# Kernel tuning notes

Measured on AMD Instinct MI355X. Metric: run time of the kernel, lower is better.

The kernel has to match this reference:

```python
import jax, jax.numpy as jnp
import numpy as np

HEADS = 8

def _rotate_every_two(t):
    # t: [..., d]; interleaved rotation (-x2, x1) pairs
    x1 = t[..., ::2]
    x2 = t[..., 1::2]
    return jnp.stack([-x2, x1], axis=-1).reshape(t.shape)

def _theta_shift(t, sin, cos):
    return t * cos + _rotate_every_two(t) * sin

def setup_inputs() -> dict:
    key = jax.random.key(0)
    ks = jax.random.split(key, 5)
    B, H, W, C = 4, 40, 40, 512
    dh = C // HEADS
    x = jax.random.normal(ks[0], (B, H, W, C), dtype=jnp.float32)
    sin = jax.random.normal(ks[1], (H, W, dh), dtype=jnp.float32)
    cos = jax.random.normal(ks[2], (H, W, dh), dtype=jnp.float32)
    # 1x1 conv weight [3C, C] (kernel dims squeezed) + bias
    w_qkv = jax.random.normal(ks[3], (3 * C, C), dtype=jnp.float32) * (C ** -0.5)
    b_qkv = jnp.zeros((3 * C,), dtype=jnp.float32)
    return {"x": x, "sin": sin, "cos": cos, "w_qkv": w_qkv, "b_qkv": b_qkv}

def reference(x, sin, cos, w_qkv, b_qkv):
    B, H, W, C = x.shape
    heads = HEADS
    dh = C // heads
    scale = dh ** -0.5
    # 1x1 conv == per-pixel linear projection
    qkv = jnp.einsum('bhwc,oc->bhwo', x, w_qkv) + b_qkv  # [B,H,W,3C]
    q, k, v = jnp.split(qkv, 3, axis=-1)

    def to_heads(t):
        # channel order is (heads, dim_head) per the torch rearrange
        return t.reshape(B, H, W, heads, dh).transpose(0, 3, 1, 2, 4)  # [B,heads,H,W,dh]

    q = _theta_shift(to_heads(q), sin, cos)
    k = _theta_shift(to_heads(k), sin, cos)
    # v is computed but unused downstream in the original module (bug preserved)

    N = H * W
    q = q.reshape(B, heads, N, dh)
    k = k.reshape(B, heads, N, dh)

    attn = jnp.einsum('bhnd,bhmd->bhnm', q, k) * scale  # [B,heads,N,N]
    p = jax.nn.softmax(attn, axis=-1)
    # NOTE: original code does matmul(logist, kfine_heads) — K, not V. Kept faithful.
    out = jnp.einsum('bhnm,bhmd->bhnd', p, k)  # [B,heads,N,dh]
    out = out.transpose(0, 2, 1, 3).reshape(B, H, W, C)
    return out
```

## Files before the change

### kernel.cpp

```cpp
#include <hip/hip_runtime.h>
#include <hip/hip_bf16.h>


typedef __hip_bfloat16 bf16;
typedef __attribute__((ext_vector_type(8))) short short8;
typedef __attribute__((ext_vector_type(4))) short bfx4;
typedef __attribute__((ext_vector_type(4))) float f32x4;

#define NSP 1600
#define CDIM 512
#define DH 64

__device__ __forceinline__ f32x4 mfma32(short8 a, short8 b, f32x4 c) {
  return __builtin_amdgcn_mfma_f32_16x16x32_bf16(a, b, c, 0, 0, 0);
}

#if __has_builtin(__builtin_amdgcn_mfma_f32_16x16x16bf16_1k)
__device__ __forceinline__ f32x4 mfma_k16(bfx4 a, bfx4 b, f32x4 c) {
  return __builtin_amdgcn_mfma_f32_16x16x16bf16_1k(a, b, c, 0, 0, 0);
}
#else
__device__ __forceinline__ f32x4 mfma_k16(bfx4 a, bfx4 b, f32x4 c) {
  short8 a8 = {a.x, a.y, a.z, a.w, 0, 0, 0, 0};
  short8 b8 = {b.x, b.y, b.z, b.w, 0, 0, 0, 0};
  return __builtin_amdgcn_mfma_f32_16x16x32_bf16(a8, b8, c, 0, 0, 0);
}
#endif

__device__ __forceinline__ short8 cvt8(float4 v0, float4 v1) {
  short8 r; bf16* p = (bf16*)&r;
  p[0] = __float2bfloat16(v0.x); p[1] = __float2bfloat16(v0.y);
  p[2] = __float2bfloat16(v0.z); p[3] = __float2bfloat16(v0.w);
  p[4] = __float2bfloat16(v1.x); p[5] = __float2bfloat16(v1.y);
  p[6] = __float2bfloat16(v1.z); p[7] = __float2bfloat16(v1.w);
  return r;
}

extern "C" __global__ __launch_bounds__(256)
void cvt_kernel(const float* __restrict__ x, const float* __restrict__ w,
                const float* __restrict__ sin_t, const float* __restrict__ cos_t,
                bf16* __restrict__ x_bf, bf16* __restrict__ w_bf,
                float* __restrict__ sinT, float* __restrict__ cosT)
{
  __shared__ float t_lds[64][68];
  const int bid = blockIdx.x, tid = threadIdx.x;
  if (bid < 1600) {
    const size_t i = (size_t)bid * 2048 + tid * 8;
    float4 v0 = *(const float4*)(x + i);
    float4 v1 = *(const float4*)(x + i + 4);
    *(short8*)(x_bf + i) = cvt8(v0, v1);
  } else if (bid < 1856) {
    const size_t i = (size_t)(bid - 1600) * 2048 + tid * 8;
    float4 v0 = *(const float4*)(w + i);
    float4 v1 = *(const float4*)(w + i + 4);
    *(short8*)(w_bf + i) = cvt8(v0, v1);
  } else {
    const int t = bid - 1856;
    const float* src = (t < 25) ? sin_t : cos_t;
    float* dst = (t < 25) ? sinT : cosT;
    const int nt = (t < 25) ? t : t - 25;
    const int r = tid >> 2, c = (tid & 3) * 16;
#pragma unroll
    for (int j = 0; j < 4; ++j)
      *(float4*)&t_lds[r][c + j * 4] =
          *(const float4*)(src + (size_t)(nt * 64 + r) * 64 + c + j * 4);
    __syncthreads();
#pragma unroll
    for (int j4 = 0; j4 < 4; ++j4) {
      float4 o;
      o.x = t_lds[c + j4 * 4 + 0][r];
      o.y = t_lds[c + j4 * 4 + 1][r];
      o.z = t_lds[c + j4 * 4 + 2][r];
      o.w = t_lds[c + j4 * 4 + 3][r];
      *(float4*)(dst + (size_t)r * NSP + nt * 64 + c + j4 * 4) = o;
    }
  }
}

extern "C" __global__ __launch_bounds__(256)
void proj_kernel(const bf16* __restrict__ x_bf, const bf16* __restrict__ w_bf,
                 const float* __restrict__ bias, const float* __restrict__ sinT,
                 const float* __restrict__ cosT, bf16* __restrict__ q_ws,
                 bf16* __restrict__ k2_ws, bf16* __restrict__ kt2_ws)
{
  __shared__ __align__(16) char smem[36864];
  bf16 (*x_lds)[72] = (bf16(*)[72])smem;
  bf16 (*w_lds)[72] = (bf16(*)[72])(smem + 18432);
  bf16* ep = (bf16*)smem;

  const int tid  = threadIdx.x;
  const int wave = tid >> 6;
  const int lane = tid & 63;
  const int col  = lane & 15;
  const int quad = lane >> 4;
  const int wm = wave >> 1, wo = wave & 1;
  const int m0 = blockIdx.x * 128;
  const int o0 = blockIdx.y * 128;

  f32x4 acc[4][4];
#pragma unroll
  for (int i = 0; i < 4; ++i)
#pragma unroll
    for (int j = 0; j < 4; ++j) acc[i][j] = {0.f, 0.f, 0.f, 0.f};

  const int srow = tid >> 1;
  const int sch  = (tid & 1) * 32;

  for (int kt = 0; kt < 8; ++kt) {
    __syncthreads();
    {
      const bf16* xs = x_bf + (size_t)(m0 + srow) * CDIM + kt * 64 + sch;
      const bf16* ws = w_bf + (size_t)(o0 + srow) * CDIM + kt * 64 + sch;
#pragma unroll
      for (int j = 0; j < 4; ++j) {
        *(short8*)&x_lds[srow][sch + j * 8] = *(const short8*)(xs + j * 8);
        *(short8*)&w_lds[srow][sch + j * 8] = *(const short8*)(ws + j * 8);
      }
    }
    __syncthreads();
#pragma unroll
    for (int half = 0; half < 2; ++half) {
      short8 af[4], bfr[4];
#pragma unroll
      for (int mt = 0; mt < 4; ++mt)
        af[mt] = *(short8*)&x_lds[wm * 64 + mt * 16 + col][half * 32 + quad * 8];
#pragma unroll
      for (int ot = 0; ot < 4; ++ot)
        bfr[ot] = *(short8*)&w_lds[wo * 64 + ot * 16 + col][half * 32 + quad * 8];
#pragma unroll
      for (int mt = 0; mt < 4; ++mt)
#pragma unroll
        for (int ot = 0; ot < 4; ++ot)
          acc[mt][ot] = mfma32(af[mt], bfr[ot], acc[mt][ot]);
    }
  }

  __syncthreads();
  const int b_idx = (m0 + wm * 64) / NSP;
  const int n0w   = m0 + wm * 64 - b_idx * NSP;
  const bool isq  = (o0 < 512);
#pragma unroll
  for (int ot = 0; ot < 4; ++ot) {
    const int o_local = wo * 64 + ot * 16 + col;
    const int o_g = o0 + o_local;
    const float bv = bias[o_g];
    const int d = o_g & 63;
#pragma unroll
    for (int mt = 0; mt < 4; ++mt) {
      const int nl = mt * 16 + quad * 4;
      float t[4], rot[4];
#pragma unroll
      for (int r = 0; r < 4; ++r) t[r] = acc[mt][ot][r] + bv;
#pragma unroll
      for (int r = 0; r < 4; ++r) {
        float tp = __shfl_xor(t[r], 1, 64);
        rot[r] = (lane & 1) ? tp : -tp;
      }
      const float4 c4 = *(const float4*)(cosT + (size_t)d * NSP + n0w + nl);
      const float4 s4 = *(const float4*)(sinT + (size_t)d * NSP + n0w + nl);
      float res[4];
      res[0] = t[0] * c4.x + rot[0] * s4.x;
      res[1] = t[1] * c4.y + rot[1] * s4.y;
      res[2] = t[2] * c4.z + rot[2] * s4.z;
      res[3] = t[3] * c4.w + rot[3] * s4.w;
      if (isq) {
#pragma unroll
        for (int r = 0; r < 4; ++r) res[r] *= 0.125f;
      }
      bfx4 pk; bf16* pp = (bf16*)&pk;
#pragma unroll
      for (int r = 0; r < 4; ++r) pp[r] = __float2bfloat16(res[r]);
      *(bfx4*)&ep[o_local * 132 + wm * 64 + nl] = pk;
    }
  }
  __syncthreads();

  if (isq) {
    const int m_l = tid >> 1, half = tid & 1;
    const int gm = m0 + m_l;
    const int bi = gm / NSP, n = gm - bi * NSP;
    const int h = (o0 >> 6) + half;
    bf16* base = q_ws + ((size_t)(bi * 8 + h) * NSP + n) * 64;
#pragma unroll
    for (int c = 0; c < 8; ++c) {
      short8 v; bf16* vp = (bf16*)&v;
#pragma unroll
      for (int j = 0; j < 8; ++j) vp[j] = ep[(half * 64 + c * 8 + j) * 132 + m_l];
      *(short8*)(base + c * 8) = v;
    }
  } else {
    const int h0 = (o0 - 512) >> 6;
#pragma unroll
    for (int it = 0; it < 8; ++it) {
      const int ci = it * 256 + tid;
      const int hh = ci >> 10, T = (ci >> 9) & 1, inner = ci & 511;
      const int ccol = inner & 15, cq = (inner >> 4) & 3;
      const int f = (inner >> 6) & 1, ti = (inner >> 7) & 1, kh2 = (inner >> 8) & 1;
      const int gmb = m0 + T * 64;
      const int bi = gmb / NSP, ktile = (gmb - bi * NSP) >> 6;
      const int m_l = T * 64 + (2 * kh2 + ti) * 16 + ccol;
      const int er0 = hh * 64 + (f * 4 + cq) * 8;
      short8 v; bf16* vp = (bf16*)&v;
#pragma unroll
      for (int j = 0; j < 8; ++j) vp[j] = ep[(er0 + j) * 132 + m_l];
      *(short8*)(k2_ws +
          (((size_t)(bi * 8 + h0 + hh) * 25 + ktile) * 512 + inner) * 8) = v;
    }
#pragma unroll
    for (int it = 0; it < 8; ++it) {
      const int ci = it * 256 + tid;
      const int hh = ci >> 10, T = (ci >> 9) & 1, inner = ci & 511;
      const int ccol = inner & 15, cq = (inner >> 4) & 3;
      const int dt = (inner >> 6) & 3, kh2 = (inner >> 8) & 1;
      const int gmb = m0 + T * 64;
      const int bi = gmb / NSP, ktile = (gmb - bi * NSP) >> 6;
      const bf16* eprow =
          ep + (hh * 64 + dt * 16 + ccol) * 132 + T * 64 + kh2 * 32 + cq * 4;
      short8 v;
      ((bfx4*)&v)[0] = *(const bfx4*)(eprow);
      ((bfx4*)&v)[1] = *(const bfx4*)(eprow + 16);
      *(short8*)(kt2_ws +
          (((size_t)(bi * 8 + h0 + hh) * 25 + ktile) * 512 + inner) * 8) = v;
    }
  }
}


#define LOADF(KF, KTF, KT)                                                    \
  {                                                                           \
    const bf16* kc_  = k2b  + (KT) * 4096;                                    \
    const bf16* kc2_ = kt2b + (KT) * 4096;                                    \
    _Pragma("unroll")                                                         \
    for (int ti = 0; ti < 2; ++ti)                                            \
      _Pragma("unroll")                                                       \
      for (int f = 0; f < 2; ++f)                                             \
        KF[ti][f] =                                                           \
            *(const short8*)(kc_ + (((kh * 2 + ti) * 2 + f) * 64 + lane) * 8);\
    _Pragma("unroll")                                                         \
    for (int dt = 0; dt < 4; ++dt)                                            \
      KTF[dt] = *(const short8*)(kc2_ + ((kh * 4 + dt) * 64 + lane) * 8);     \
  }

#define COMPUTEF(KF, KTF)                                                     \
  {                                                                           \
    f32x4 s[2][2];                                                            \
    _Pragma("unroll")                                                         \
    for (int ti = 0; ti < 2; ++ti)                                            \
      _Pragma("unroll")                                                       \
      for (int ct = 0; ct < 2; ++ct) {                                        \
        f32x4 t = {0.f, 0.f, 0.f, 0.f};                                       \
        t = mfma32(KF[ti][0], qb[ct][0], t);                                  \
        t = mfma32(KF[ti][1], qb[ct][1], t);                                  \
        s[ti][ct] = t;                                                        \
      }                                                                       \
    bfx4 p4[2][2];                                                            \
    _Pragma("unroll")                                                         \
    for (int ti = 0; ti < 2; ++ti)                                            \
      _Pragma("unroll")                                                       \
      for (int ct = 0; ct < 2; ++ct) {                                        \
        _Pragma("unroll")                                                     \
        for (int r = 0; r < 4; ++r) s[ti][ct][r] = __expf(s[ti][ct][r]);      \
        l_part[ct] +=                                                         \
            s[ti][ct][0] + s[ti][ct][1] + s[ti][ct][2] + s[ti][ct][3];        \
        bf16* pp = (bf16*)&p4[ti][ct];                                        \
        _Pragma("unroll")                                                     \
        for (int r = 0; r < 4; ++r) pp[r] = __float2bfloat16(s[ti][ct][r]);   \
      }                                                                       \
    _Pragma("unroll")                                                         \
    for (int dt = 0; dt < 4; ++dt) {                                          \
      bfx4 alo = __builtin_shufflevector(KTF[dt], KTF[dt], 0, 1, 2, 3);       \
      bfx4 ahi = __builtin_shufflevector(KTF[dt], KTF[dt], 4, 5, 6, 7);       \
      _Pragma("unroll")                                                       \
      for (int ct = 0; ct < 2; ++ct) {                                        \
        oacc[dt][ct] = mfma_k16(alo, p4[0][ct], oacc[dt][ct]);                \
        oacc[dt][ct] = mfma_k16(ahi, p4[1][ct], oacc[dt][ct]);                \
      }                                                                       \
    }                                                                         \
  }

extern "C" __global__ __launch_bounds__(256, 2)
void attn_kernel(const bf16* __restrict__ q_ws, const bf16* __restrict__ k2_ws,
                 const bf16* __restrict__ kt2_ws, float* __restrict__ out)
{
  __shared__ float red[2][64][36];

  const int id = blockIdx.x;
  const int xr = id & 7, inner = id >> 3;
  const int qt = inner % 25;
  const int bh = (inner / 25) * 8 + xr;
  const int b = bh >> 3, h = bh & 7;
  const int tid  = threadIdx.x;
  const int wave = tid >> 6;
  const int lane = tid & 63;
  const int col  = lane & 15;
  const int quad = lane >> 4;
  const int qg = wave & 1, kh = wave >> 1;

  short8 qb[2][2];
#pragma unroll
  for (int ct = 0; ct < 2; ++ct) {
    const bf16* qp =
        q_ws + ((size_t)bh * NSP + qt * 64 + (qg * 2 + ct) * 16 + col) * 64;
    qb[ct][0] = *(const short8*)(qp + quad * 8);
    qb[ct][1] = *(const short8*)(qp + 32 + quad * 8);
  }

  f32x4 oacc[4][2];
#pragma unroll
  for (int i = 0; i < 4; ++i)
#pragma unroll
    for (int j = 0; j < 2; ++j) oacc[i][j] = {0.f, 0.f, 0.f, 0.f};
  float l_part[2] = {0.f, 0.f};

  const bf16* k2b  = k2_ws  + (size_t)bh * 25 * 4096;
  const bf16* kt2b = kt2_ws + (size_t)bh * 25 * 4096;

  short8 kfA[2][2], ktfA[4], kfB[2][2], ktfB[4];
  LOADF(kfA, ktfA, 0)
#pragma unroll 1
  for (int i = 0; i < 12; ++i) {
    LOADF(kfB, ktfB, 2 * i + 1)
    COMPUTEF(kfA, ktfA)
    LOADF(kfA, ktfA, 2 * i + 2)
    COMPUTEF(kfB, ktfB)
  }
  COMPUTEF(kfA, ktfA)

#pragma unroll
  for (int ct = 0; ct < 2; ++ct) {
    l_part[ct] += __shfl_xor(l_part[ct], 16, 64);
    l_part[ct] += __shfl_xor(l_part[ct], 32, 64);
  }

  if (wave >= 2) {
    float* dst = &red[wave - 2][lane][0];
#pragma unroll
    for (int dt = 0; dt < 4; ++dt)
#pragma unroll
      for (int ct = 0; ct < 2; ++ct)
        *(f32x4*)(dst + (dt * 2 + ct) * 4) = oacc[dt][ct];
    dst[32] = l_part[0]; dst[33] = l_part[1];
  }
  __syncthreads();
  if (wave < 2) {
    const float* srcr = &red[wave][lane][0];
#pragma unroll
    for (int dt = 0; dt < 4; ++dt)
#pragma unroll
      for (int ct = 0; ct < 2; ++ct)
        oacc[dt][ct] += *(const f32x4*)(srcr + (dt * 2 + ct) * 4);
    const float inv0 = 1.f / (l_part[0] + srcr[32]);
    const float inv1 = 1.f / (l_part[1] + srcr[33]);
#pragma unroll
    for (int ct = 0; ct < 2; ++ct) {
      const float inv = ct ? inv1 : inv0;
      const int qrow = qt * 64 + (qg * 2 + ct) * 16 + col;
      float* ob = out + ((size_t)b * NSP + qrow) * CDIM + h * 64;
#pragma unroll
      for (int dt = 0; dt < 4; ++dt) {
        float4 v;
        v.x = oacc[dt][ct][0] * inv; v.y = oacc[dt][ct][1] * inv;
        v.z = oacc[dt][ct][2] * inv; v.w = oacc[dt][ct][3] * inv;
        *(float4*)(ob + dt * 16 + quad * 4) = v;
      }
    }
  }
}

extern "C" void kernel_launch(void* const* d_in, const int* in_sizes, int n_in,
                              void* d_out, int out_size, void* d_ws, size_t ws_size,
                              hipStream_t stream) {
  const float* x     = (const float*)d_in[0];
  const float* sin_t = (const float*)d_in[1];
  const float* cos_t = (const float*)d_in[2];
  const float* w_qkv = (const float*)d_in[3];
  const float* b_qkv = (const float*)d_in[4];
  float* out = (float*)d_out;

  const size_t QK = (size_t)32 * NSP * DH;
  bf16* q_ws   = (bf16*)d_ws;
  bf16* k2_ws  = q_ws + QK;
  bf16* kt2_ws = k2_ws + QK;
  bf16* x_bf   = kt2_ws + QK;
  bf16* w_bf   = x_bf + (size_t)6400 * CDIM;
  float* sinT  = (float*)(w_bf + (size_t)1024 * CDIM);
  float* cosT  = sinT + (size_t)DH * NSP;

  cvt_kernel<<<1906, 256, 0, stream>>>(x, w_qkv, sin_t, cos_t, x_bf, w_bf, sinT, cosT);

  dim3 gproj(50, 8);
  proj_kernel<<<gproj, 256, 0, stream>>>(x_bf, w_bf, b_qkv, sinT, cosT,
                                         q_ws, k2_ws, kt2_ws);

  attn_kernel<<<800, 256, 0, stream>>>(q_ws, k2_ws, kt2_ws, out);
}
```

Before: 136.7 us.

## Split key tiles across four waves, each covering all 64 query rows

Changes the work split inside the attention block. Previously waves were arranged 2 query groups × 2 key halves; now each of the 4 waves owns one 16-key quarter of every key tile and computes scores for all 64 query rows. Each wave loads half as much K data per tile and issues one K16 MFMA per (dt, ct) pair, so K fragments are reused across more query columns. The cost is a larger accumulator footprint per wave (16 f32x4 plus 4 sums) and a bigger three-way LDS reduction that wave 0 performs alone at the end.

```diff
diff --git a/kernel.cpp b/kernel.cpp
--- a/kernel.cpp
+++ b/kernel.cpp
@@ -230,59 +230,46 @@
   {                                                                           \
     const bf16* kc_  = k2b  + (KT) * 4096;                                    \
     const bf16* kc2_ = kt2b + (KT) * 4096;                                    \
-    _Pragma("unroll")                                                         \
-    for (int ti = 0; ti < 2; ++ti)                                            \
-      _Pragma("unroll")                                                       \
-      for (int f = 0; f < 2; ++f)                                             \
-        KF[ti][f] =                                                           \
-            *(const short8*)(kc_ + (((kh * 2 + ti) * 2 + f) * 64 + lane) * 8);\
+    KF[0] = *(const short8*)(kc_ + ((kh * 2 + 0) * 64 + lane) * 8);           \
+    KF[1] = *(const short8*)(kc_ + ((kh * 2 + 1) * 64 + lane) * 8);           \
     _Pragma("unroll")                                                         \
     for (int dt = 0; dt < 4; ++dt)                                            \
-      KTF[dt] = *(const short8*)(kc2_ + ((kh * 4 + dt) * 64 + lane) * 8);     \
+      KTF[dt] =                                                               \
+          *(const bfx4*)(kc2_ + ((khh * 4 + dt) * 64 + lane) * 8 + khl * 4);  \
   }
 
 #define COMPUTEF(KF, KTF)                                                     \
   {                                                                           \
-    f32x4 s[2][2];                                                            \
+    f32x4 s[4];                                                               \
     _Pragma("unroll")                                                         \
-    for (int ti = 0; ti < 2; ++ti)                                            \
+    for (int ct = 0; ct < 4; ++ct) {                                          \
+      f32x4 t = {0.f, 0.f, 0.f, 0.f};                                         \
+      t = mfma32(KF[0], qb[ct][0], t);                                        \
+      t = mfma32(KF[1], qb[ct][1], t);                                        \
+      s[ct] = t;                                                              \
+    }                                                                         \
+    bfx4 p4[4];                                                               \
+    _Pragma("unroll")                                                         \
+    for (int ct = 0; ct < 4; ++ct) {                                          \
       _Pragma("unroll")                                                       \
-      for (int ct = 0; ct < 2; ++ct) {                                        \
-        f32x4 t = {0.f, 0.f, 0.f, 0.f};                                       \
-        t = mfma32(KF[ti][0], qb[ct][0], t);                                  \
-        t = mfma32(KF[ti][1], qb[ct][1], t);                                  \
-        s[ti][ct] = t;                                                        \
-      }                                                                       \
-    bfx4 p4[2][2];                                                            \
+      for (int r = 0; r < 4; ++r) s[ct][r] = __expf(s[ct][r]);                \
+      l_part[ct] += s[ct][0] + s[ct][1] + s[ct][2] + s[ct][3];                \
+      bf16* pp = (bf16*)&p4[ct];                                              \
+      _Pragma("unroll")                                                       \
+      for (int r = 0; r < 4; ++r) pp[r] = __float2bfloat16(s[ct][r]);         \
+    }                                                                         \
     _Pragma("unroll")                                                         \
-    for (int ti = 0; ti < 2; ++ti)                                            \
+    for (int dt = 0; dt < 4; ++dt)                                            \
       _Pragma("unroll")                                                       \
-      for (int ct = 0; ct < 2; ++ct) {                                        \
-        _Pragma("unroll")                                                     \
-        for (int r = 0; r < 4; ++r) s[ti][ct][r] = __expf(s[ti][ct][r]);      \
-        l_part[ct] +=                                                         \
-            s[ti][ct][0] + s[ti][ct][1] + s[ti][ct][2] + s[ti][ct][3];        \
-        bf16* pp = (bf16*)&p4[ti][ct];                                        \
-        _Pragma("unroll")                                                     \
-        for (int r = 0; r < 4; ++r) pp[r] = __float2bfloat16(s[ti][ct][r]);   \
-      }                                                                       \
-    _Pragma("unroll")                                                         \
-    for (int dt = 0; dt < 4; ++dt) {                                          \
-      bfx4 alo = __builtin_shufflevector(KTF[dt], KTF[dt], 0, 1, 2, 3);       \
-      bfx4 ahi = __builtin_shufflevector(KTF[dt], KTF[dt], 4, 5, 6, 7);       \
-      _Pragma("unroll")                                                       \
-      for (int ct = 0; ct < 2; ++ct) {                                        \
-        oacc[dt][ct] = mfma_k16(alo, p4[0][ct], oacc[dt][ct]);                \
-        oacc[dt][ct] = mfma_k16(ahi, p4[1][ct], oacc[dt][ct]);                \
-      }                                                                       \
-    }                                                                         \
+      for (int ct = 0; ct < 4; ++ct)                                          \
+        oacc[dt][ct] = mfma_k16(KTF[dt], p4[ct], oacc[dt][ct]);               \
   }
 
 extern "C" __global__ __launch_bounds__(256, 2)
 void attn_kernel(const bf16* __restrict__ q_ws, const bf16* __restrict__ k2_ws,
                  const bf16* __restrict__ kt2_ws, float* __restrict__ out)
 {
-  __shared__ float red[2][64][36];
+  __shared__ float red[3][64][69];
 
   const int id = blockIdx.x;
   const int xr = id & 7, inner = id >> 3;
@@ -294,28 +281,30 @@
   const int lane = tid & 63;
   const int col  = lane & 15;
   const int quad = lane >> 4;
-  const int qg = wave & 1, kh = wave >> 1;
-
-  short8 qb[2][2];
-#pragma unroll
-  for (int ct = 0; ct < 2; ++ct) {
+  const int kh = wave;
+  const int khh = kh >> 1, khl = kh & 1;
+
+  short8 qb[4][2];
+#pragma unroll
+  for (int ct = 0; ct < 4; ++ct) {
     const bf16* qp =
-        q_ws + ((size_t)bh * NSP + qt * 64 + (qg * 2 + ct) * 16 + col) * 64;
+        q_ws + ((size_t)bh * NSP + qt * 64 + ct * 16 + col) * 64;
     qb[ct][0] = *(const short8*)(qp + quad * 8);
     qb[ct][1] = *(const short8*)(qp + 32 + quad * 8);
   }
 
-  f32x4 oacc[4][2];
+  f32x4 oacc[4][4];
 #pragma unroll
   for (int i = 0; i < 4; ++i)
 #pragma unroll
-    for (int j = 0; j < 2; ++j) oacc[i][j] = {0.f, 0.f, 0.f, 0.f};
-  float l_part[2] = {0.f, 0.f};
+    for (int j = 0; j < 4; ++j) oacc[i][j] = {0.f, 0.f, 0.f, 0.f};
+  float l_part[4] = {0.f, 0.f, 0.f, 0.f};
 
   const bf16* k2b  = k2_ws  + (size_t)bh * 25 * 4096;
   const bf16* kt2b = kt2_ws + (size_t)bh * 25 * 4096;
 
-  short8 kfA[2][2], ktfA[4], kfB[2][2], ktfB[4];
+  short8 kfA[2], kfB[2];
+  bfx4 ktfA[4], ktfB[4];
   LOADF(kfA, ktfA, 0)
 #pragma unroll 1
   for (int i = 0; i < 12; ++i) {
@@ -327,34 +316,38 @@
   COMPUTEF(kfA, ktfA)
 
 #pragma unroll
-  for (int ct = 0; ct < 2; ++ct) {
+  for (int ct = 0; ct < 4; ++ct) {
     l_part[ct] += __shfl_xor(l_part[ct], 16, 64);
     l_part[ct] += __shfl_xor(l_part[ct], 32, 64);
   }
 
-  if (wave >= 2) {
-    float* dst = &red[wave - 2][lane][0];
+  if (wave >= 1) {
+    float* dst = &red[wave - 1][lane][0];
 #pragma unroll
     for (int dt = 0; dt < 4; ++dt)
 #pragma unroll
-      for (int ct = 0; ct < 2; ++ct)
-        *(f32x4*)(dst + (dt * 2 + ct) * 4) = oacc[dt][ct];
-    dst[32] = l_part[0]; dst[33] = l_part[1];
+      for (int ct = 0; ct < 4; ++ct)
+        *(f32x4*)(dst + (dt * 4 + ct) * 4) = oacc[dt][ct];
+#pragma unroll
+    for (int ct = 0; ct < 4; ++ct) dst[64 + ct] = l_part[ct];
   }
   __syncthreads();
-  if (wave < 2) {
-    const float* srcr = &red[wave][lane][0];
-#pragma unroll
-    for (int dt = 0; dt < 4; ++dt)
-#pragma unroll
-      for (int ct = 0; ct < 2; ++ct)
-        oacc[dt][ct] += *(const f32x4*)(srcr + (dt * 2 + ct) * 4);
-    const float inv0 = 1.f / (l_part[0] + srcr[32]);
-    const float inv1 = 1.f / (l_part[1] + srcr[33]);
-#pragma unroll
-    for (int ct = 0; ct < 2; ++ct) {
-      const float inv = ct ? inv1 : inv0;
-      const int qrow = qt * 64 + (qg * 2 + ct) * 16 + col;
+  if (wave == 0) {
+#pragma unroll
+    for (int w = 0; w < 3; ++w) {
+      const float* srcr = &red[w][lane][0];
+#pragma unroll
+      for (int dt = 0; dt < 4; ++dt)
+#pragma unroll
+        for (int ct = 0; ct < 4; ++ct)
+          oacc[dt][ct] += *(const f32x4*)(srcr + (dt * 4 + ct) * 4);
+#pragma unroll
+      for (int ct = 0; ct < 4; ++ct) l_part[ct] += srcr[64 + ct];
+    }
+#pragma unroll
+    for (int ct = 0; ct < 4; ++ct) {
+      const float inv = 1.f / l_part[ct];
+      const int qrow = qt * 64 + ct * 16 + col;
       float* ob = out + ((size_t)b * NSP + qrow) * CDIM + h * 64;
 #pragma unroll
       for (int dt = 0; dt < 4; ++dt) {
```

After: 141.8 us. 1.04x slower.

## Fuse fp32-to-bf16 conversion into projection GEMM with double-buffered LDS

Applied to the files above, without the earlier changes.

The separate conversion pass for x and w_qkv is removed. The projection kernel now loads fp32 tiles straight from global memory, converts them to bf16 in registers, and writes them into one of two LDS buffers. It prefetches the next k-tile while the current one feeds the MFMAs, which drops one barrier per iteration. This saves a kernel launch and the round trip through bf16 workspace, at the cost of reading fp32 (twice the bytes) in the GEMM, more registers, and 72KB of LDS with launch_bounds(256,1).

```diff
diff --git a/kernel.cpp b/kernel.cpp
--- a/kernel.cpp
+++ b/kernel.cpp
@@ -37,55 +37,42 @@
 }
 
 extern "C" __global__ __launch_bounds__(256)
-void cvt_kernel(const float* __restrict__ x, const float* __restrict__ w,
-                const float* __restrict__ sin_t, const float* __restrict__ cos_t,
-                bf16* __restrict__ x_bf, bf16* __restrict__ w_bf,
+void cvt_kernel(const float* __restrict__ sin_t, const float* __restrict__ cos_t,
                 float* __restrict__ sinT, float* __restrict__ cosT)
 {
   __shared__ float t_lds[64][68];
-  const int bid = blockIdx.x, tid = threadIdx.x;
-  if (bid < 1600) {
-    const size_t i = (size_t)bid * 2048 + tid * 8;
-    float4 v0 = *(const float4*)(x + i);
-    float4 v1 = *(const float4*)(x + i + 4);
-    *(short8*)(x_bf + i) = cvt8(v0, v1);
-  } else if (bid < 1856) {
-    const size_t i = (size_t)(bid - 1600) * 2048 + tid * 8;
-    float4 v0 = *(const float4*)(w + i);
-    float4 v1 = *(const float4*)(w + i + 4);
-    *(short8*)(w_bf + i) = cvt8(v0, v1);
-  } else {
-    const int t = bid - 1856;
-    const float* src = (t < 25) ? sin_t : cos_t;
-    float* dst = (t < 25) ? sinT : cosT;
-    const int nt = (t < 25) ? t : t - 25;
-    const int r = tid >> 2, c = (tid & 3) * 16;
-#pragma unroll
-    for (int j = 0; j < 4; ++j)
-      *(float4*)&t_lds[r][c + j * 4] =
-          *(const float4*)(src + (size_t)(nt * 64 + r) * 64 + c + j * 4);
-    __syncthreads();
-#pragma unroll
-    for (int j4 = 0; j4 < 4; ++j4) {
-      float4 o;
-      o.x = t_lds[c + j4 * 4 + 0][r];
-      o.y = t_lds[c + j4 * 4 + 1][r];
-      o.z = t_lds[c + j4 * 4 + 2][r];
-      o.w = t_lds[c + j4 * 4 + 3][r];
-      *(float4*)(dst + (size_t)r * NSP + nt * 64 + c + j4 * 4) = o;
-    }
-  }
-}
-
-extern "C" __global__ __launch_bounds__(256)
-void proj_kernel(const bf16* __restrict__ x_bf, const bf16* __restrict__ w_bf,
+  const int t = blockIdx.x, tid = threadIdx.x;
+  const float* src = (t < 25) ? sin_t : cos_t;
+  float* dst = (t < 25) ? sinT : cosT;
+  const int nt = (t < 25) ? t : t - 25;
+  const int r = tid >> 2, c = (tid & 3) * 16;
+#pragma unroll
+  for (int j = 0; j < 4; ++j)
+    *(float4*)&t_lds[r][c + j * 4] =
+        *(const float4*)(src + (size_t)(nt * 64 + r) * 64 + c + j * 4);
+  __syncthreads();
+#pragma unroll
+  for (int j4 = 0; j4 < 4; ++j4) {
+    float4 o;
+    o.x = t_lds[c + j4 * 4 + 0][r];
+    o.y = t_lds[c + j4 * 4 + 1][r];
+    o.z = t_lds[c + j4 * 4 + 2][r];
+    o.w = t_lds[c + j4 * 4 + 3][r];
+    *(float4*)(dst + (size_t)r * NSP + nt * 64 + c + j4 * 4) = o;
+  }
+}
+
+extern "C" __global__ __launch_bounds__(256, 1)
+void proj_kernel(const float* __restrict__ x, const float* __restrict__ w,
                  const float* __restrict__ bias, const float* __restrict__ sinT,
                  const float* __restrict__ cosT, bf16* __restrict__ q_ws,
                  bf16* __restrict__ k2_ws, bf16* __restrict__ kt2_ws)
 {
-  __shared__ __align__(16) char smem[36864];
-  bf16 (*x_lds)[72] = (bf16(*)[72])smem;
-  bf16 (*w_lds)[72] = (bf16(*)[72])(smem + 18432);
+  __shared__ __align__(16) char smem[73728];
+  bf16 (*xl0)[72] = (bf16(*)[72])smem;
+  bf16 (*wl0)[72] = (bf16(*)[72])(smem + 18432);
+  bf16 (*xl1)[72] = (bf16(*)[72])(smem + 36864);
+  bf16 (*wl1)[72] = (bf16(*)[72])(smem + 55296);
   bf16* ep = (bf16*)smem;
 
   const int tid  = threadIdx.x;
@@ -105,37 +92,60 @@
 
   const int srow = tid >> 1;
   const int sch  = (tid & 1) * 32;
-
+  const float* xs_base = x + (size_t)(m0 + srow) * CDIM + sch;
+  const float* ws_base = w + (size_t)(o0 + srow) * CDIM + sch;
+
+  float4 xr[8], wr[8];
+#pragma unroll
+  for (int j = 0; j < 8; ++j) xr[j] = *(const float4*)(xs_base + j * 4);
+#pragma unroll
+  for (int j = 0; j < 8; ++j) wr[j] = *(const float4*)(ws_base + j * 4);
+#pragma unroll
+  for (int j = 0; j < 4; ++j) {
+    *(short8*)&xl0[srow][sch + j * 8] = cvt8(xr[2 * j], xr[2 * j + 1]);
+    *(short8*)&wl0[srow][sch + j * 8] = cvt8(wr[2 * j], wr[2 * j + 1]);
+  }
+  __syncthreads();
+
+#pragma unroll
   for (int kt = 0; kt < 8; ++kt) {
-    __syncthreads();
-    {
-      const bf16* xs = x_bf + (size_t)(m0 + srow) * CDIM + kt * 64 + sch;
-      const bf16* ws = w_bf + (size_t)(o0 + srow) * CDIM + kt * 64 + sch;
-#pragma unroll
-      for (int j = 0; j < 4; ++j) {
-        *(short8*)&x_lds[srow][sch + j * 8] = *(const short8*)(xs + j * 8);
-        *(short8*)&w_lds[srow][sch + j * 8] = *(const short8*)(ws + j * 8);
-      }
-    }
-    __syncthreads();
+    if (kt < 7) {
+#pragma unroll
+      for (int j = 0; j < 8; ++j)
+        xr[j] = *(const float4*)(xs_base + (kt + 1) * 64 + j * 4);
+#pragma unroll
+      for (int j = 0; j < 8; ++j)
+        wr[j] = *(const float4*)(ws_base + (kt + 1) * 64 + j * 4);
+    }
+    bf16 (*xl)[72] = (kt & 1) ? xl1 : xl0;
+    bf16 (*wl)[72] = (kt & 1) ? wl1 : wl0;
 #pragma unroll
     for (int half = 0; half < 2; ++half) {
       short8 af[4], bfr[4];
 #pragma unroll
       for (int mt = 0; mt < 4; ++mt)
-        af[mt] = *(short8*)&x_lds[wm * 64 + mt * 16 + col][half * 32 + quad * 8];
+        af[mt] = *(short8*)&xl[wm * 64 + mt * 16 + col][half * 32 + quad * 8];
 #pragma unroll
       for (int ot = 0; ot < 4; ++ot)
-        bfr[ot] = *(short8*)&w_lds[wo * 64 + ot * 16 + col][half * 32 + quad * 8];
+        bfr[ot] = *(short8*)&wl[wo * 64 + ot * 16 + col][half * 32 + quad * 8];
 #pragma unroll
       for (int mt = 0; mt < 4; ++mt)
 #pragma unroll
         for (int ot = 0; ot < 4; ++ot)
           acc[mt][ot] = mfma32(af[mt], bfr[ot], acc[mt][ot]);
     }
-  }
-
-  __syncthreads();
+    if (kt < 7) {
+      bf16 (*xn)[72] = (kt & 1) ? xl0 : xl1;
+      bf16 (*wn)[72] = (kt & 1) ? wl0 : wl1;
+#pragma unroll
+      for (int j = 0; j < 4; ++j) {
+        *(short8*)&xn[srow][sch + j * 8] = cvt8(xr[2 * j], xr[2 * j + 1]);
+        *(short8*)&wn[srow][sch + j * 8] = cvt8(wr[2 * j], wr[2 * j + 1]);
+      }
+    }
+    __syncthreads();
+  }
+
   const int b_idx = (m0 + wm * 64) / NSP;
   const int n0w   = m0 + wm * 64 - b_idx * NSP;
   const bool isq  = (o0 < 512);
@@ -381,15 +391,13 @@
   bf16* q_ws   = (bf16*)d_ws;
   bf16* k2_ws  = q_ws + QK;
   bf16* kt2_ws = k2_ws + QK;
-  bf16* x_bf   = kt2_ws + QK;
-  bf16* w_bf   = x_bf + (size_t)6400 * CDIM;
-  float* sinT  = (float*)(w_bf + (size_t)1024 * CDIM);
+  float* sinT  = (float*)(kt2_ws + QK);
   float* cosT  = sinT + (size_t)DH * NSP;
 
-  cvt_kernel<<<1906, 256, 0, stream>>>(x, w_qkv, sin_t, cos_t, x_bf, w_bf, sinT, cosT);
+  cvt_kernel<<<50, 256, 0, stream>>>(sin_t, cos_t, sinT, cosT);
 
   dim3 gproj(50, 8);
-  proj_kernel<<<gproj, 256, 0, stream>>>(x_bf, w_bf, b_qkv, sinT, cosT,
+  proj_kernel<<<gproj, 256, 0, stream>>>(x, w_qkv, b_qkv, sinT, cosT,
                                          q_ws, k2_ws, kt2_ws);
 
   attn_kernel<<<800, 256, 0, stream>>>(q_ws, k2_ws, kt2_ws, out);
```

New measurement: 157.6 us. 1.15x slower.

## Load projection GEMM operands directly from global memory, bypassing LDS staging

Applied to the files above, without the earlier changes.

The projection GEMM no longer stages x and w tiles through shared memory with barriers. Each lane instead loads its MFMA fragments straight from global memory, and the k loop is fully unrolled. The grid becomes 1D with the output tile index fastest and launch bounds set to one block, and the shared buffer shrinks to what the epilogue needs. This removes LDS round trips and __syncthreads, at the cost of more global or L2 traffic, since each fragment is reloaded by several waves, and less latency hiding.

```diff
diff --git a/kernel.cpp b/kernel.cpp
--- a/kernel.cpp
+++ b/kernel.cpp
@@ -77,15 +77,13 @@
   }
 }
 
-extern "C" __global__ __launch_bounds__(256)
+extern "C" __global__ __launch_bounds__(256, 1)
 void proj_kernel(const bf16* __restrict__ x_bf, const bf16* __restrict__ w_bf,
                  const float* __restrict__ bias, const float* __restrict__ sinT,
                  const float* __restrict__ cosT, bf16* __restrict__ q_ws,
                  bf16* __restrict__ k2_ws, bf16* __restrict__ kt2_ws)
 {
-  __shared__ __align__(16) char smem[36864];
-  bf16 (*x_lds)[72] = (bf16(*)[72])smem;
-  bf16 (*w_lds)[72] = (bf16(*)[72])(smem + 18432);
+  __shared__ __align__(16) char smem[33792];
   bf16* ep = (bf16*)smem;
 
   const int tid  = threadIdx.x;
@@ -94,8 +92,9 @@
   const int col  = lane & 15;
   const int quad = lane >> 4;
   const int wm = wave >> 1, wo = wave & 1;
-  const int m0 = blockIdx.x * 128;
-  const int o0 = blockIdx.y * 128;
+  const int id = blockIdx.x;
+  const int m0 = (id >> 3) * 128;
+  const int o0 = (id & 7) * 128;
 
   f32x4 acc[4][4];
 #pragma unroll
@@ -103,30 +102,21 @@
 #pragma unroll
     for (int j = 0; j < 4; ++j) acc[i][j] = {0.f, 0.f, 0.f, 0.f};
 
-  const int srow = tid >> 1;
-  const int sch  = (tid & 1) * 32;
-
+  const bf16* xb = x_bf + ((size_t)(m0 + wm * 64 + col) << 9) + quad * 8;
+  const bf16* wb = w_bf + ((size_t)(o0 + wo * 64 + col) << 9) + quad * 8;
+
+#pragma unroll
   for (int kt = 0; kt < 8; ++kt) {
-    __syncthreads();
-    {
-      const bf16* xs = x_bf + (size_t)(m0 + srow) * CDIM + kt * 64 + sch;
-      const bf16* ws = w_bf + (size_t)(o0 + srow) * CDIM + kt * 64 + sch;
-#pragma unroll
-      for (int j = 0; j < 4; ++j) {
-        *(short8*)&x_lds[srow][sch + j * 8] = *(const short8*)(xs + j * 8);
-        *(short8*)&w_lds[srow][sch + j * 8] = *(const short8*)(ws + j * 8);
-      }
-    }
-    __syncthreads();
 #pragma unroll
     for (int half = 0; half < 2; ++half) {
+      const int c0 = kt * 64 + half * 32;
       short8 af[4], bfr[4];
 #pragma unroll
       for (int mt = 0; mt < 4; ++mt)
-        af[mt] = *(short8*)&x_lds[wm * 64 + mt * 16 + col][half * 32 + quad * 8];
+        af[mt] = *(const short8*)(xb + ((size_t)mt << 13) + c0);
 #pragma unroll
       for (int ot = 0; ot < 4; ++ot)
-        bfr[ot] = *(short8*)&w_lds[wo * 64 + ot * 16 + col][half * 32 + quad * 8];
+        bfr[ot] = *(const short8*)(wb + ((size_t)ot << 13) + c0);
 #pragma unroll
       for (int mt = 0; mt < 4; ++mt)
 #pragma unroll
@@ -135,7 +125,6 @@
     }
   }
 
-  __syncthreads();
   const int b_idx = (m0 + wm * 64) / NSP;
   const int n0w   = m0 + wm * 64 - b_idx * NSP;
   const bool isq  = (o0 < 512);
@@ -388,9 +377,8 @@
 
   cvt_kernel<<<1906, 256, 0, stream>>>(x, w_qkv, sin_t, cos_t, x_bf, w_bf, sinT, cosT);
 
-  dim3 gproj(50, 8);
-  proj_kernel<<<gproj, 256, 0, stream>>>(x_bf, w_bf, b_qkv, sinT, cosT,
-                                         q_ws, k2_ws, kt2_ws);
+  proj_kernel<<<400, 256, 0, stream>>>(x_bf, w_bf, b_qkv, sinT, cosT,
+                                       q_ws, k2_ws, kt2_ws);
 
   attn_kernel<<<800, 256, 0, stream>>>(q_ws, k2_ws, kt2_ws, out);
 }
```

New measurement: 151.8 us. 11.1% more time.
